# Performance work log

Hardware: AMD Instinct MI355X
Metric: run time of the kernel (lower is better)

## Reference

```python
import jax, jax.numpy as jnp
import numpy as np

IN_FEATURES = 4096
OUT_FEATURES = 4096
GROUPS = 1
QB = 2 ** (8 - 1) - 1  # 127, int8 absmax quant


def setup_inputs() -> dict:
    key = jax.random.key(0)
    k_x, k_w = jax.random.split(key)
    x = jax.random.normal(k_x, (8192, IN_FEATURES), dtype=jnp.float32)
    # kaiming_uniform_(a=sqrt(5)) -> uniform(-1/sqrt(in), 1/sqrt(in))
    bound = 1.0 / np.sqrt(IN_FEATURES)
    weight = jax.random.uniform(
        k_w, (OUT_FEATURES, IN_FEATURES), dtype=jnp.float32,
        minval=-bound, maxval=bound)
    return {"input": x, "weight": weight}


def reference(input, weight):
    # --- ternarize weight per group ---
    w = weight.reshape(GROUPS, -1)                       # [G, out*in/G]
    w = w - jnp.mean(w, axis=1, keepdims=True)
    w = jnp.sign(w)
    # beta: per-group scale (note denominator uses full element count, as in source)
    beta = jnp.sum(jnp.abs(w), axis=1, keepdims=True) / (w.shape[0] * w.shape[1])
    w = (w * beta).reshape(OUT_FEATURES, IN_FEATURES)    # [out, in]

    # --- absmax int8 quantize activations (quantized values used, not dequant) ---
    scale = QB / jnp.max(jnp.abs(input))
    quant = jnp.round(scale * input)                     # [tokens, in]

    # --- linear + rescale ---
    out = quant @ w.T                                    # [tokens, out]
    out = out / beta.reshape(-1, 1)                      # groups=1: scalar divide
    return out
```

## Files before the change

### kernel.cpp

```cpp
#include <hip/hip_runtime.h>
#include <hip/hip_bf16.h>

typedef __attribute__((ext_vector_type(4))) int int4v;

#define TOKENS 8192
#define IN_F   4096
#define OUT_F  4096


__global__ __launch_bounds__(256) void k_pre(const float4* __restrict__ w,
                                             const float4* __restrict__ x,
                                             double* __restrict__ partials,
                                             float* __restrict__ xpart) {
  if (blockIdx.x < 1024) {
    __shared__ double sm[256];
    double s = 0.0;
    const float4* p = w + (size_t)blockIdx.x * 4096;
    for (int i = threadIdx.x; i < 4096; i += 256) {
      float4 v = p[i];
      s += (double)v.x + (double)v.y + (double)v.z + (double)v.w;
    }
    sm[threadIdx.x] = s;
    __syncthreads();
    for (int off = 128; off > 0; off >>= 1) {
      if (threadIdx.x < off) sm[threadIdx.x] += sm[threadIdx.x + off];
      __syncthreads();
    }
    if (threadIdx.x == 0) partials[blockIdx.x] = sm[0];
  } else {
    const int b = blockIdx.x - 1024;
    float m = 0.f;
    const size_t n = (size_t)TOKENS * IN_F / 4;
    for (size_t i = (size_t)b * 256 + threadIdx.x; i < n; i += (size_t)1024 * 256) {
      float4 v = x[i];
      m = fmaxf(m, fmaxf(fmaxf(fabsf(v.x), fabsf(v.y)),
                         fmaxf(fabsf(v.z), fabsf(v.w))));
    }
    __shared__ float smf[256];
    smf[threadIdx.x] = m;
    __syncthreads();
    for (int off = 128; off > 0; off >>= 1) {
      if (threadIdx.x < off) smf[threadIdx.x] = fmaxf(smf[threadIdx.x], smf[threadIdx.x + off]);
      __syncthreads();
    }
    if (threadIdx.x == 0) xpart[b] = smf[0];
  }
}

__global__ __launch_bounds__(256) void k_finalize(double* __restrict__ hdr,
                                                  const double* __restrict__ partials,
                                                  const float* __restrict__ xpart) {
  __shared__ double sm[256];
  __shared__ float smf[256];
  double s = partials[threadIdx.x] + partials[threadIdx.x + 256] +
             partials[threadIdx.x + 512] + partials[threadIdx.x + 768];
  float m = fmaxf(fmaxf(xpart[threadIdx.x], xpart[threadIdx.x + 256]),
                  fmaxf(xpart[threadIdx.x + 512], xpart[threadIdx.x + 768]));
  sm[threadIdx.x] = s;
  smf[threadIdx.x] = m;
  __syncthreads();
  for (int off = 128; off > 0; off >>= 1) {
    if (threadIdx.x < off) {
      sm[threadIdx.x] += sm[threadIdx.x + off];
      smf[threadIdx.x] = fmaxf(smf[threadIdx.x], smf[threadIdx.x + off]);
    }
    __syncthreads();
  }
  if (threadIdx.x == 0) {
    hdr[0] = sm[0] / (double)((size_t)OUT_F * IN_F);
    hdr[1] = 127.0 / (double)smf[0];
  }
}

#define QB_BLK ((TOKENS * IN_F / 4) / 256)
#define TB_BLK ((OUT_F * IN_F / 4) / 256)
__global__ __launch_bounds__(256) void k_quant_tern(const float4* __restrict__ x,
                                                    const float4* __restrict__ w,
                                                    int* __restrict__ q,
                                                    int* __restrict__ sgn,
                                                    const double* __restrict__ hdr) {
  if (blockIdx.x < QB_BLK) {
    const double s = hdr[1];
    size_t i = (size_t)blockIdx.x * 256 + threadIdx.x;
    float4 v = x[i];
    int a = (int)rint(s * (double)v.x);
    int b = (int)rint(s * (double)v.y);
    int c = (int)rint(s * (double)v.z);
    int d = (int)rint(s * (double)v.w);
    q[i] = (a & 255) | ((b & 255) << 8) | ((c & 255) << 16) | ((d & 255) << 24);
  } else {
    const double m = hdr[0];
    size_t i = (size_t)(blockIdx.x - QB_BLK) * 256 + threadIdx.x;
    float4 v = w[i];
    int a = ((double)v.x > m) - ((double)v.x < m);
    int b = ((double)v.y > m) - ((double)v.y < m);
    int c = ((double)v.z > m) - ((double)v.z < m);
    int d = ((double)v.w > m) - ((double)v.w < m);
    sgn[i] = (a & 255) | ((b & 255) << 8) | ((c & 255) << 16) | ((d & 255) << 24);
  }
}

__global__ __launch_bounds__(512, 2) void k_gemm(const signed char* __restrict__ q,
                                                 const signed char* __restrict__ s,
                                                 float* __restrict__ out) {
  __shared__ signed char sA[4][256 * 64];
  __shared__ signed char sB[4][256 * 64];
  const int tid  = threadIdx.x;
  const int lane = tid & 63;
  const int wid  = tid >> 6;
  const int wm   = wid >> 2;
  const int wn   = wid & 3;
  const int l15  = lane & 15, l4 = lane >> 4;

  const int swz = (blockIdx.x & 7) * 64 + (blockIdx.x >> 3);
  const int bm = swz >> 4;
  const int bn = swz & 15;
  const size_t row0 = (size_t)bm * 256;
  const size_t col0 = (size_t)bn * 256;

  const int lane_off = l15 * 64 + ((l4 ^ ((l15 >> 1) & 3)) << 4);

#define STAGE_A(KT, BUF)                                                        \
  do {                                                                          \
    const int kt_ = (KT);                                                       \
    _Pragma("unroll")                                                           \
    for (int u = 0; u < 2; ++u) {                                               \
      const int slot = u * 512 + tid;                                           \
      const int r = slot >> 2, sir = slot & 3;                                  \
      const int koff = ((sir ^ ((r >> 1) & 3)) << 4);                           \
      __builtin_amdgcn_global_load_lds(                                         \
          (const __attribute__((address_space(1))) void*)(q + (row0 + (size_t)r) * IN_F + kt_ * 64 + koff), \
          (__attribute__((address_space(3))) void*)(sA[BUF] + (u * 512 + wid * 64) * 16), 16, 0, 0); \
    }                                                                           \
  } while (0)

#define STAGE_B(KT, BUF)                                                        \
  do {                                                                          \
    const int kt_ = (KT);                                                       \
    _Pragma("unroll")                                                           \
    for (int u = 0; u < 2; ++u) {                                               \
      const int slot = u * 512 + tid;                                           \
      const int r = slot >> 2, sir = slot & 3;                                  \
      const int koff = ((sir ^ ((r >> 1) & 3)) << 4);                           \
      __builtin_amdgcn_global_load_lds(                                         \
          (const __attribute__((address_space(1))) void*)(s + (col0 + (size_t)r) * IN_F + kt_ * 64 + koff), \
          (__attribute__((address_space(3))) void*)(sB[BUF] + (u * 512 + wid * 64) * 16), 16, 0, 0); \
    }                                                                           \
  } while (0)

#define READ_A8(BUF, AV)                                                        \
  do {                                                                          \
    _Pragma("unroll")                                                           \
    for (int f = 0; f < 8; ++f)                                                 \
      AV[f] = *(const int4v*)(sA[BUF] + (wm * 128 + f * 16) * 64 + lane_off);   \
  } while (0)

#define READ_B01(BUF)                                                           \
  do {                                                                          \
    b01[0] = *(const int4v*)(sB[BUF] + (wn * 64 +  0) * 64 + lane_off);         \
    b01[1] = *(const int4v*)(sB[BUF] + (wn * 64 + 16) * 64 + lane_off);         \
  } while (0)

#define READ_B23(BUF)                                                           \
  do {                                                                          \
    b23[0] = *(const int4v*)(sB[BUF] + (wn * 64 + 32) * 64 + lane_off);         \
    b23[1] = *(const int4v*)(sB[BUF] + (wn * 64 + 48) * 64 + lane_off);         \
  } while (0)

#define MFMA16(AV, BV, NB)                                                      \
  do {                                                                          \
    _Pragma("unroll")                                                           \
    for (int m_ = 0; m_ < 8; ++m_) {                                            \
      acc[m_][NB]     = __builtin_amdgcn_mfma_i32_16x16x64_i8(AV[m_], BV[0],    \
                                                              acc[m_][NB], 0, 0, 0); \
      acc[m_][NB + 1] = __builtin_amdgcn_mfma_i32_16x16x64_i8(AV[m_], BV[1],    \
                                                              acc[m_][NB + 1], 0, 0, 0); \
    }                                                                           \
  } while (0)

#define SB0() __builtin_amdgcn_sched_barrier(0)

#define PHASE0(KT, RB, SBUF, AC)                                                \
  do {                                                                          \
    READ_B23(RB);                                                               \
    STAGE_A(((KT) + 3) & 63, SBUF);                                             \
    SB0();                                                                      \
    __builtin_amdgcn_s_barrier();                                               \
    asm volatile("s_waitcnt lgkmcnt(2)" ::: "memory");                          \
    SB0();                                                                      \
    __builtin_amdgcn_s_setprio(1);                                              \
    MFMA16(AC, b01, 0);                                                         \
    __builtin_amdgcn_s_setprio(0);                                              \
    SB0();                                                                      \
    asm volatile("s_waitcnt vmcnt(6)" ::: "memory");                            \
    SB0();                                                                      \
    __builtin_amdgcn_s_barrier();                                               \
    SB0();                                                                      \
  } while (0)

#define PHASE1(KT, NB, SBUF, AC, AN)                                            \
  do {                                                                          \
    READ_A8(NB, AN);                                                            \
    READ_B01(NB);                                                               \
    STAGE_B(((KT) + 3) & 63, SBUF);                                             \
    SB0();                                                                      \
    __builtin_amdgcn_s_barrier();                                               \
    asm volatile("s_waitcnt lgkmcnt(10)" ::: "memory");                         \
    SB0();                                                                      \
    __builtin_amdgcn_s_setprio(1);                                              \
    MFMA16(AC, b23, 2);                                                         \
    __builtin_amdgcn_s_setprio(0);                                              \
    SB0();                                                                      \
    __builtin_amdgcn_s_barrier();                                               \
    SB0();                                                                      \
  } while (0)

  int4v acc[8][4];
#pragma unroll
  for (int i = 0; i < 8; ++i)
#pragma unroll
    for (int j = 0; j < 4; ++j) acc[i][j] = int4v{0, 0, 0, 0};

  int4v aX[8], aY[8], b01[2], b23[2];

  STAGE_A(0, 0); STAGE_B(0, 0);
  STAGE_A(1, 1); STAGE_B(1, 1);
  STAGE_A(2, 2); STAGE_B(2, 2);
  SB0();
  asm volatile("s_waitcnt vmcnt(8)" ::: "memory");
  __builtin_amdgcn_s_barrier();
  SB0();
  READ_A8(0, aX);
  READ_B01(0);
  SB0();

  for (int kt = 0; kt < 64; kt += 4) {
    PHASE0(kt + 0, 0, 3, aX);  PHASE1(kt + 0, 1, 3, aX, aY);
    PHASE0(kt + 1, 1, 0, aY);  PHASE1(kt + 1, 2, 0, aY, aX);
    PHASE0(kt + 2, 2, 1, aX);  PHASE1(kt + 2, 3, 1, aX, aY);
    PHASE0(kt + 3, 3, 2, aY);  PHASE1(kt + 3, 0, 2, aY, aX);
  }

#pragma unroll
  for (int m = 0; m < 8; ++m)
#pragma unroll
    for (int n = 0; n < 4; ++n)
#pragma unroll
      for (int r = 0; r < 4; ++r) {
        const size_t rg = row0 + wm * 128 + m * 16 + l4 * 4 + r;
        const size_t cg = col0 + wn * 64 + n * 16 + l15;
        out[rg * OUT_F + cg] = (float)acc[m][n][r];
      }

#undef STAGE_A
#undef STAGE_B
#undef READ_A8
#undef READ_B01
#undef READ_B23
#undef MFMA16
#undef PHASE0
#undef PHASE1
#undef SB0
}

extern "C" void kernel_launch(void* const* d_in, const int* in_sizes, int n_in,
                              void* d_out, int out_size, void* d_ws, size_t ws_size,
                              hipStream_t stream) {
  const float* x = (const float*)d_in[0];
  const float* w = (const float*)d_in[1];
  float* out = (float*)d_out;

  char* ws = (char*)d_ws;
  double*   hdr      = (double*)ws;
  double*   partials = (double*)(ws + 1024);
  float*    xpart    = (float*)(ws + 9216);
  signed char* qbuf  = (signed char*)(ws + 16384);
  signed char* sbuf  = (signed char*)(ws + 16384 + (size_t)TOKENS * IN_F);

  k_pre<<<2048, 256, 0, stream>>>((const float4*)w, (const float4*)x, partials, xpart);
  k_finalize<<<1, 256, 0, stream>>>(hdr, partials, xpart);
  k_quant_tern<<<QB_BLK + TB_BLK, 256, 0, stream>>>((const float4*)x, (const float4*)w,
                                                    (int*)qbuf, (int*)sbuf, hdr);
  k_gemm<<<(TOKENS / 256) * (OUT_F / 256), 512, 0, stream>>>(qbuf, sbuf, out);
}
```

Measured before the change: 223.4 us.

## Merge two-phase GEMM loop into one barrier-per-k-tile body with full register double buffer

Replaces the two half-phase iterations per k-tile (each with two barriers and split B-fragment reads) with a single body per k-tile. Each body waits, passes one barrier, reads all A and B fragments for the next tile into a second register set, issues the combined A+B global-to-LDS prefetch, then runs all 32 MFMAs. This halves the barrier count and simplifies waitcnt bookkeeping. In exchange it holds a full extra set of B fragments in registers and gives the scheduler coarser interleaving of LDS reads, global prefetch and MFMA work.

```diff
diff --git a/kernel.cpp b/kernel.cpp
--- a/kernel.cpp
+++ b/kernel.cpp
@@ -120,7 +120,9 @@
 
   const int lane_off = l15 * 64 + ((l4 ^ ((l15 >> 1) & 3)) << 4);
 
-#define STAGE_A(KT, BUF)                                                        \
+#define SB0() __builtin_amdgcn_sched_barrier(0)
+
+#define STAGE_AB(KT, BUF)                                                       \
   do {                                                                          \
     const int kt_ = (KT);                                                       \
     _Pragma("unroll")                                                           \
@@ -128,91 +130,58 @@
       const int slot = u * 512 + tid;                                           \
       const int r = slot >> 2, sir = slot & 3;                                  \
       const int koff = ((sir ^ ((r >> 1) & 3)) << 4);                           \
+      const int ldst = (u * 512 + wid * 64) * 16;                               \
       __builtin_amdgcn_global_load_lds(                                         \
           (const __attribute__((address_space(1))) void*)(q + (row0 + (size_t)r) * IN_F + kt_ * 64 + koff), \
-          (__attribute__((address_space(3))) void*)(sA[BUF] + (u * 512 + wid * 64) * 16), 16, 0, 0); \
+          (__attribute__((address_space(3))) void*)(sA[BUF] + ldst), 16, 0, 0); \
     }                                                                           \
-  } while (0)
-
-#define STAGE_B(KT, BUF)                                                        \
-  do {                                                                          \
-    const int kt_ = (KT);                                                       \
     _Pragma("unroll")                                                           \
     for (int u = 0; u < 2; ++u) {                                               \
       const int slot = u * 512 + tid;                                           \
       const int r = slot >> 2, sir = slot & 3;                                  \
       const int koff = ((sir ^ ((r >> 1) & 3)) << 4);                           \
+      const int ldst = (u * 512 + wid * 64) * 16;                               \
       __builtin_amdgcn_global_load_lds(                                         \
           (const __attribute__((address_space(1))) void*)(s + (col0 + (size_t)r) * IN_F + kt_ * 64 + koff), \
-          (__attribute__((address_space(3))) void*)(sB[BUF] + (u * 512 + wid * 64) * 16), 16, 0, 0); \
+          (__attribute__((address_space(3))) void*)(sB[BUF] + ldst), 16, 0, 0); \
     }                                                                           \
   } while (0)
 
-#define READ_A8(BUF, AV)                                                        \
+#define READ12(BUF, AV, BV)                                                     \
   do {                                                                          \
     _Pragma("unroll")                                                           \
     for (int f = 0; f < 8; ++f)                                                 \
       AV[f] = *(const int4v*)(sA[BUF] + (wm * 128 + f * 16) * 64 + lane_off);   \
-  } while (0)
-
-#define READ_B01(BUF)                                                           \
-  do {                                                                          \
-    b01[0] = *(const int4v*)(sB[BUF] + (wn * 64 +  0) * 64 + lane_off);         \
-    b01[1] = *(const int4v*)(sB[BUF] + (wn * 64 + 16) * 64 + lane_off);         \
-  } while (0)
-
-#define READ_B23(BUF)                                                           \
-  do {                                                                          \
-    b23[0] = *(const int4v*)(sB[BUF] + (wn * 64 + 32) * 64 + lane_off);         \
-    b23[1] = *(const int4v*)(sB[BUF] + (wn * 64 + 48) * 64 + lane_off);         \
-  } while (0)
-
-#define MFMA16(AV, BV, NB)                                                      \
-  do {                                                                          \
-    _Pragma("unroll")                                                           \
-    for (int m_ = 0; m_ < 8; ++m_) {                                            \
-      acc[m_][NB]     = __builtin_amdgcn_mfma_i32_16x16x64_i8(AV[m_], BV[0],    \
-                                                              acc[m_][NB], 0, 0, 0); \
-      acc[m_][NB + 1] = __builtin_amdgcn_mfma_i32_16x16x64_i8(AV[m_], BV[1],    \
-                                                              acc[m_][NB + 1], 0, 0, 0); \
-    }                                                                           \
-  } while (0)
-
-#define SB0() __builtin_amdgcn_sched_barrier(0)
-
-#define PHASE0(KT, RB, SBUF, AC)                                                \
-  do {                                                                          \
-    READ_B23(RB);                                                               \
-    STAGE_A(((KT) + 3) & 63, SBUF);                                             \
+    _Pragma("unroll")                                                           \
+    for (int f = 0; f < 4; ++f)                                                 \
+      BV[f] = *(const int4v*)(sB[BUF] + (wn * 64 + f * 16) * 64 + lane_off);    \
+  } while (0)
+
+#define MFMA32(AV, BV)                                                          \
+  do {                                                                          \
+    _Pragma("unroll")                                                           \
+    for (int m_ = 0; m_ < 8; ++m_)                                              \
+      _Pragma("unroll")                                                         \
+      for (int n_ = 0; n_ < 4; ++n_)                                            \
+        acc[m_][n_] = __builtin_amdgcn_mfma_i32_16x16x64_i8(AV[m_], BV[n_],     \
+                                                            acc[m_][n_], 0, 0, 0); \
+  } while (0)
+
+#define BODY(KT, RBUF, SBUF, ACUR, BCUR, ANXT, BNXT)                            \
+  do {                                                                          \
+    asm volatile("s_waitcnt vmcnt(4)" ::: "memory");                            \
     SB0();                                                                      \
     __builtin_amdgcn_s_barrier();                                               \
-    asm volatile("s_waitcnt lgkmcnt(2)" ::: "memory");                          \
+    SB0();                                                                      \
+    READ12(RBUF, ANXT, BNXT);                                                   \
+    STAGE_AB(((KT) + 3) & 63, SBUF);                                            \
+    SB0();                                                                      \
+    asm volatile("s_waitcnt lgkmcnt(12)" ::: "memory");                         \
     SB0();                                                                      \
     __builtin_amdgcn_s_setprio(1);                                              \
-    MFMA16(AC, b01, 0);                                                         \
+    MFMA32(ACUR, BCUR);                                                         \
     __builtin_amdgcn_s_setprio(0);                                              \
     SB0();                                                                      \
-    asm volatile("s_waitcnt vmcnt(6)" ::: "memory");                            \
-    SB0();                                                                      \
-    __builtin_amdgcn_s_barrier();                                               \
-    SB0();                                                                      \
-  } while (0)
-
-#define PHASE1(KT, NB, SBUF, AC, AN)                                            \
-  do {                                                                          \
-    READ_A8(NB, AN);                                                            \
-    READ_B01(NB);                                                               \
-    STAGE_B(((KT) + 3) & 63, SBUF);                                             \
-    SB0();                                                                      \
-    __builtin_amdgcn_s_barrier();                                               \
-    asm volatile("s_waitcnt lgkmcnt(10)" ::: "memory");                         \
-    SB0();                                                                      \
-    __builtin_amdgcn_s_setprio(1);                                              \
-    MFMA16(AC, b23, 2);                                                         \
-    __builtin_amdgcn_s_setprio(0);                                              \
-    SB0();                                                                      \
-    __builtin_amdgcn_s_barrier();                                               \
-    SB0();                                                                      \
   } while (0)
 
   int4v acc[8][4];
@@ -221,24 +190,24 @@
 #pragma unroll
     for (int j = 0; j < 4; ++j) acc[i][j] = int4v{0, 0, 0, 0};
 
-  int4v aX[8], aY[8], b01[2], b23[2];
-
-  STAGE_A(0, 0); STAGE_B(0, 0);
-  STAGE_A(1, 1); STAGE_B(1, 1);
-  STAGE_A(2, 2); STAGE_B(2, 2);
+  int4v aX[8], bX[4], aY[8], bY[4];
+
+  STAGE_AB(0, 0);
+  STAGE_AB(1, 1);
+  STAGE_AB(2, 2);
   SB0();
   asm volatile("s_waitcnt vmcnt(8)" ::: "memory");
+  SB0();
   __builtin_amdgcn_s_barrier();
   SB0();
-  READ_A8(0, aX);
-  READ_B01(0);
+  READ12(0, aX, bX);
   SB0();
 
   for (int kt = 0; kt < 64; kt += 4) {
-    PHASE0(kt + 0, 0, 3, aX);  PHASE1(kt + 0, 1, 3, aX, aY);
-    PHASE0(kt + 1, 1, 0, aY);  PHASE1(kt + 1, 2, 0, aY, aX);
-    PHASE0(kt + 2, 2, 1, aX);  PHASE1(kt + 2, 3, 1, aX, aY);
-    PHASE0(kt + 3, 3, 2, aY);  PHASE1(kt + 3, 0, 2, aY, aX);
+    BODY(kt + 0, 1, 3, aX, bX, aY, bY);
+    BODY(kt + 1, 2, 0, aY, bY, aX, bX);
+    BODY(kt + 2, 3, 1, aX, bX, aY, bY);
+    BODY(kt + 3, 0, 2, aY, bY, aX, bX);
   }
 
 #pragma unroll
@@ -252,15 +221,11 @@
         out[rg * OUT_F + cg] = (float)acc[m][n][r];
       }
 
-#undef STAGE_A
-#undef STAGE_B
-#undef READ_A8
-#undef READ_B01
-#undef READ_B23
-#undef MFMA16
-#undef PHASE0
-#undef PHASE1
 #undef SB0
+#undef STAGE_AB
+#undef READ12
+#undef MFMA32
+#undef BODY
 }
 
 extern "C" void kernel_launch(void* const* d_in, const int* in_sizes, int n_in,
```

After: 227.1 us. Within noise of the previous version (+1.7%).
